# Kernel optimization log

Hardware: AMD Instinct MI355X
Metric: run time of the kernel (lower is better)

The kernel has to match this reference:

```python
import jax, jax.numpy as jnp
import numpy as np

S, B, H, D, G = 2048, 2, 16, 128, 16  # seq, batch, heads, head_dim, v-quant groups


def setup_inputs() -> dict:
    key = jax.random.key(0)
    ks = jax.random.split(key, 9)
    # int8-valued activations stored as float (torch code does .to(torch.int8))
    q = jax.random.randint(ks[0], (S, B, H, D), -128, 128).astype(jnp.float32)
    k = jax.random.randint(ks[1], (S, B, H, D), -128, 128).astype(jnp.float32)
    v = jax.random.randint(ks[2], (S, B, H, D), -128, 128).astype(jnp.float32)
    qmin = jax.random.normal(ks[3], (S, B, H, 1), jnp.float32) * 0.01
    qscale = jax.random.uniform(ks[4], (S, B, H, 1), jnp.float32, 0.005, 0.02)
    kmin = jax.random.normal(ks[5], (S, B, H, 1), jnp.float32) * 0.01
    kscale = jax.random.uniform(ks[6], (S, B, H, 1), jnp.float32, 0.005, 0.02)
    vmin = jax.random.normal(ks[7], (G, B, H, D, 1), jnp.float32) * 0.01
    vscale = jax.random.uniform(ks[8], (G, B, H, D, 1), jnp.float32, 0.005, 0.02)
    return {"query_layer": q, "key_layer": k, "value_layer": v,
            "qmin": qmin, "qscale": qscale, "kmin": kmin, "kscale": kscale,
            "vmin": vmin, "vscale": vscale, "causal": 1}


def _attention(query_layer, key_layer, value_layer, qmin, qscale, kmin, kscale, vmin, vscale, causal):
    # s b h d -> b h s d ; emulate .to(torch.int8) (values are already int8-range ints)
    q = jnp.transpose(query_layer, (1, 2, 0, 3))
    k = jnp.transpose(key_layer, (1, 2, 0, 3))
    v = jnp.transpose(value_layer, (1, 2, 0, 3))
    # per-token quant factors: s b h 1 -> b h s 1
    qm = jnp.transpose(qmin[..., 0], (1, 2, 0))[..., None]
    qs = jnp.transpose(qscale[..., 0], (1, 2, 0))[..., None]
    km = jnp.transpose(kmin[..., 0], (1, 2, 0))[..., None]
    ksc = jnp.transpose(kscale[..., 0], (1, 2, 0))[..., None]
    # attnq_qk: dequantize per-token then QK^T
    qd = q * qs + qm
    kd = k * ksc + km
    scores = jnp.einsum('bhsd,bhtd->bhst', qd, kd)
    # softmaxq: scale by 1/sqrt(128), causal mask, softmax, int8 requant of probs
    scores = scores * jnp.float32(1.0 / np.sqrt(128.0))
    s = scores.shape[-1]
    if causal:
        mask = jnp.tril(jnp.ones((s, s), dtype=bool))
        scores = jnp.where(mask, scores, jnp.float32(-1e9))
    probs = jax.nn.softmax(scores, axis=-1)
    pmin = jnp.min(probs, axis=-1, keepdims=True)
    pmax = jnp.max(probs, axis=-1, keepdims=True)
    pscale = (pmax - pmin) / 255.0 + jnp.float32(1e-12)
    quant_prob = jnp.round((probs - pmin) / pscale)  # int8-range prob codes
    # attnq_pv: dequant probs (per query token) and V (per sequence group) then PV
    pd = quant_prob * pscale + pmin
    vm = jnp.transpose(vmin[..., 0], (1, 2, 0, 3))  # b h g d
    vs = jnp.transpose(vscale[..., 0], (1, 2, 0, 3))
    gs = v.shape[2] // vm.shape[2]  # group size along sequence
    vd = v * jnp.repeat(vs, gs, axis=2) + jnp.repeat(vm, gs, axis=2)
    out = jnp.einsum('bhst,bhtd->bhsd', pd, vd)
    b, h, sq, d = out.shape
    return jnp.transpose(out, (2, 0, 1, 3)).reshape(sq, b, h * d)  # s b (h d)


def reference(query_layer, key_layer, value_layer, qmin, qscale, kmin, kscale, vmin, vscale, causal):
    return _attention(query_layer, key_layer, value_layer, qmin, qscale, kmin, kscale, vmin, vscale, causal)
```

## Files before the change

kernel.cpp:

```cpp
#include <hip/hip_runtime.h>
#include <math.h>


#define S_LEN 2048
#define BATCH 2
#define NH    16
#define HD    128
#define RSTR  4096
#define SCALE2 (0.08838834764831845f * 1.4426950408889634f)
#define EXP2F(x) __builtin_amdgcn_exp2f(x)

typedef int v4i __attribute__((ext_vector_type(4)));
#define MFMA16(a,b,c) __builtin_amdgcn_mfma_i32_16x16x64_i8((a),(b),(c),0,0,0)

#define WS_K8   0u
#define WS_V8T  (8u*1024u*1024u)
#define WS_SQ   (16u*1024u*1024u)
#define WS_SK   (WS_SQ + 256u*1024u)
#define WS_GSV  (WS_SK + 256u*1024u)

__device__ __forceinline__ int sbsum(unsigned p) {
    return (int)(signed char)(p) + (int)(signed char)(p>>8)
         + (int)(signed char)(p>>16) + (int)(signed char)(p>>24);
}

__global__ __launch_bounds__(256) void prep_pack(
    const float* __restrict__ Q, const float* __restrict__ K, const float* __restrict__ V,
    signed char* __restrict__ K8, float* __restrict__ SQs, float* __restrict__ SKs,
    signed char* __restrict__ V8T, float* __restrict__ GSV)
{
    __shared__ int v8i[128*33];
    const int tid = threadIdx.x;
    const int bx  = blockIdx.x;
    if (bx >= 512) {
        const int base = (bx - 512)*256 + tid;
        #pragma unroll
        for (int rep = 0; rep < 8; ++rep) {
            const int tensor = rep >> 2;
            const int idx = base + (rep & 3)*524288;
            const float* src = tensor ? K : Q;
            int tau = idx >> 5, dg = idx & 31;
            float4 x = *(const float4*)(src + (size_t)tau*128 + 4*dg);
            float ssum = x.x + x.y + x.z + x.w;
            #pragma unroll
            for (int off = 16; off >= 1; off >>= 1) ssum += __shfl_xor(ssum, off);
            if (tensor) {
                int a=(int)x.x, b2=(int)x.y, c=(int)x.z, d=(int)x.w;
                ((int*)K8)[(size_t)tau*32 + dg] = (a&255)|((b2&255)<<8)|((c&255)<<16)|((d&255)<<24);
                if ((tid & 31) == 0) SKs[tau] = ssum;
            } else {
                if ((tid & 31) == 0) SQs[tau] = ssum;
            }
        }
    } else {
        const int bid = bx;
        const int bh = bid & 31, ck = bid >> 5;
        const int b = bh >> 4, h = bh & 15;
        const int t0 = ck * 128;
        const int boff = b*2048 + h*128;
        #pragma unroll
        for (int it = 0; it < 16; ++it) {
            int idx = tid + it*256;
            int t = idx >> 5, dw = idx & 31;
            float4 x = *(const float4*)(V + (size_t)(t0+t)*RSTR + boff + 4*dw);
            int a=(int)x.x, b2=(int)x.y, c=(int)x.z, d=(int)x.w;
            v8i[t*33 + dw] = (a&255)|((b2&255)<<8)|((c&255)<<16)|((d&255)<<24);
        }
        __syncthreads();
        #pragma unroll
        for (int it = 0; it < 4; ++it) {
            int j = tid + it*256;
            int tg = j & 31, dw = j >> 5;
            unsigned r0 = (unsigned)v8i[(4*tg+0)*33 + dw];
            unsigned r1 = (unsigned)v8i[(4*tg+1)*33 + dw];
            unsigned r2 = (unsigned)v8i[(4*tg+2)*33 + dw];
            unsigned r3 = (unsigned)v8i[(4*tg+3)*33 + dw];
            unsigned x01 = __builtin_amdgcn_perm(r1, r0, 0x05010400u);
            unsigned x23 = __builtin_amdgcn_perm(r3, r2, 0x05010400u);
            unsigned y01 = __builtin_amdgcn_perm(r1, r0, 0x07030602u);
            unsigned y23 = __builtin_amdgcn_perm(r3, r2, 0x07030602u);
            unsigned p[4];
            p[0] = __builtin_amdgcn_perm(x23, x01, 0x05040100u);
            p[1] = __builtin_amdgcn_perm(x23, x01, 0x07060302u);
            p[2] = __builtin_amdgcn_perm(y23, y01, 0x05040100u);
            p[3] = __builtin_amdgcn_perm(y23, y01, 0x07060302u);
            int s[4];
            #pragma unroll
            for (int jj = 0; jj < 4; ++jj) {
                int d = 4*dw + jj;
                *(int*)(V8T + ((size_t)bh*128 + d)*2048 + t0 + 4*tg) = (int)p[jj];
                s[jj] = sbsum(p[jj]);
            }
            #pragma unroll
            for (int off = 1; off < 32; off <<= 1) {
                #pragma unroll
                for (int jj = 0; jj < 4; ++jj) s[jj] += __shfl_xor(s[jj], off);
            }
            if (tg == 0) {
                #pragma unroll
                for (int jj = 0; jj < 4; ++jj)
                    GSV[((size_t)bh*16 + ck)*128 + 4*dw + jj] = (float)s[jj];
            }
        }
    }
}

__global__ __launch_bounds__(256, 2) void attn_main(
    const float* __restrict__ Q,
    const signed char* __restrict__ K8, const signed char* __restrict__ V8T,
    const float* __restrict__ QMN, const float* __restrict__ QSC,
    const float* __restrict__ KMN, const float* __restrict__ KSC,
    const float* __restrict__ VMN, const float* __restrict__ VSC,
    const float* __restrict__ SQs, const float* __restrict__ SKs,
    const float* __restrict__ GSV,
    const int* __restrict__ CAUSAL, float* __restrict__ OUT)
{
    __shared__ __align__(16) signed char q8s[64*144];
    __shared__ __align__(16) signed char kv8s[128*144];
    __shared__ __align__(16) signed char pcs[64*144];
    __shared__ float rs_c1[64], rs_c2[64], rs_c3[64];
    __shared__ float rs_mx[64], rs_den[64], rs_mn[64];
    __shared__ float rs_u1[64], rs_w1[64], rs_psc[64], rs_pmn[64];
    __shared__ float ktA[2][128], ktB[2][128], ktC[2][128];
    __shared__ float vsA[128], vsB[128];
    __shared__ float vsumL[128], cgsL[128];

    signed char* k8s = kv8s;
    signed char* v8s = kv8s;

    const int tid  = threadIdx.x;
    const int w    = tid >> 6;
    const int lane = tid & 63;
    const int n    = lane & 15;
    const int quad = lane >> 4;
    const int bhi  = blockIdx.x & 31;
    const int qt   = 31 - (int)(blockIdx.x >> 5);
    const int b    = bhi >> 4, h = bhi & 15;
    const int causal = *CAUSAL;
    const int s0   = qt * 64;
    const int boff = b*2048 + h*128;
    const v4i vzero = {0,0,0,0};
    const v4i ones  = {0x01010101,0x01010101,0x01010101,0x01010101};

    #pragma unroll
    for (int it = 0; it < 8; ++it) {
        int idx = tid + it*256;
        int row = idx >> 5, d4 = (idx & 31) << 2;
        float4 x = *(const float4*)(Q + (size_t)(s0+row)*RSTR + boff + d4);
        int a=(int)x.x, b2=(int)x.y, c=(int)x.z, d=(int)x.w;
        *(int*)(q8s + row*144 + d4) = (a&255)|((b2&255)<<8)|((c&255)<<16)|((d&255)<<24);
    }
    if (tid < 64) {
        int si = (s0 + tid)*32 + bhi;
        float qs = QSC[si], qm = QMN[si];
        rs_c1[tid] = qs; rs_c2[tid] = qm;
        rs_c3[tid] = fmaf(qs, SQs[si], 128.0f*qm);
    }
    __syncthreads();

    const int kt_end = causal ? ((s0 + 63) >> 7) : 15;

    float c1r[4], c2r[4], c3r[4]; int qgr[4];
    #pragma unroll
    for (int r = 0; r < 4; ++r) {
        int qq = 16*w + 4*quad + r;
        c1r[r] = rs_c1[qq]; c2r[r] = rs_c2[qq]; c3r[r] = rs_c3[qq];
        qgr[r] = s0 + qq;
    }
    v4i a0p = *(const v4i*)(q8s + (16*w + n)*144 + 16*quad);
    v4i a1p = *(const v4i*)(q8s + (16*w + n)*144 + 64 + 16*quad);

    float m[4], l[4], mn[4];
    #pragma unroll
    for (int r = 0; r < 4; ++r) { m[r] = -INFINITY; l[r] = 0.f; mn[r] = INFINITY; }

#define P1_TILE(MASKED)                                                          \
  do {                                                                           \
    const int t0g = kt * 128;                                                    \
    __syncthreads();                                                             \
    _Pragma("unroll")                                                            \
    for (int it = 0; it < 4; ++it) {                                             \
        int idx = tid + it*256;                                                  \
        int trow = idx >> 3, doff = (idx & 7) << 4;                              \
        *(uint4*)(k8s + trow*144 + doff) =                                       \
            *(const uint4*)(K8 + ((size_t)(t0g+trow)*32 + bhi)*128 + doff);      \
    }                                                                            \
    if (tid < 128) {                                                             \
        int si = (t0g + tid)*32 + bhi;                                           \
        ktA[0][tid] = KSC[si]*SCALE2; ktB[0][tid] = KMN[si]*SCALE2;              \
        ktC[0][tid] = SKs[si];                                                   \
    }                                                                            \
    __syncthreads();                                                             \
    float tmax[4], sarr[8][4];                                                   \
    _Pragma("unroll")                                                            \
    for (int r = 0; r < 4; ++r) tmax[r] = -INFINITY;                             \
    _Pragma("unroll")                                                            \
    for (int tb = 0; tb < 8; ++tb) {                                             \
        v4i b0 = *(const v4i*)(k8s + (16*tb + n)*144 + 16*quad);                 \
        v4i b1 = *(const v4i*)(k8s + (16*tb + n)*144 + 64 + 16*quad);            \
        v4i acc = MFMA16(a0p, b0, vzero);                                        \
        acc = MFMA16(a1p, b1, acc);                                              \
        int tl = 16*tb + n;                                                      \
        float kA = ktA[0][tl], kB = ktB[0][tl], kC = ktC[0][tl];                 \
        _Pragma("unroll")                                                        \
        for (int r = 0; r < 4; ++r) {                                            \
            float Sf = (float)acc[r];                                            \
            float sv = fmaf(kA, fmaf(c1r[r], Sf, c2r[r]*kC), kB*c3r[r]);         \
            if (MASKED) sv = (t0g + tl > qgr[r]) ? -INFINITY : sv;               \
            sarr[tb][r] = sv;                                                    \
            tmax[r] = fmaxf(tmax[r], sv);                                        \
            mn[r] = fminf(mn[r], sv);                                            \
        }                                                                        \
    }                                                                            \
    _Pragma("unroll")                                                            \
    for (int r = 0; r < 4; ++r) {                                                \
        float mm = fmaxf(m[r], tmax[r]);                                         \
        if (mm > -INFINITY) {                                                    \
            float e0 = EXP2F(sarr[0][r]-mm) + EXP2F(sarr[1][r]-mm);              \
            float e1 = EXP2F(sarr[2][r]-mm) + EXP2F(sarr[3][r]-mm);              \
            float e2 = EXP2F(sarr[4][r]-mm) + EXP2F(sarr[5][r]-mm);              \
            float e3 = EXP2F(sarr[6][r]-mm) + EXP2F(sarr[7][r]-mm);              \
            l[r] = fmaf(l[r], EXP2F(m[r]-mm), (e0+e1)+(e2+e3));                  \
            m[r] = mm;                                                           \
        }                                                                        \
    }                                                                            \
  } while (0)

    {
        int kt;
        for (kt = 0; kt < kt_end; ++kt) P1_TILE(false);
        kt = kt_end;
        if (causal) P1_TILE(true); else P1_TILE(false);
    }

    #pragma unroll
    for (int r = 0; r < 4; ++r) {
        #pragma unroll
        for (int off = 1; off < 16; off <<= 1) {
            float m2 = __shfl_xor(m[r], off);
            float l2 = __shfl_xor(l[r], off);
            float n2 = __shfl_xor(mn[r], off);
            float mm = fmaxf(m[r], m2);
            if (mm > -INFINITY) l[r] = l[r]*EXP2F(m[r]-mm) + l2*EXP2F(m2-mm);
            m[r] = mm;
            mn[r] = fminf(mn[r], n2);
        }
        if (n == 0) {
            int qq = 16*w + 4*quad + r;
            rs_mx[qq] = m[r]; rs_den[qq] = l[r]; rs_mn[qq] = mn[r];
        }
    }
    __syncthreads();
    if (tid < 64) {
        float mx = rs_mx[tid], den = rs_den[tid], mnv = rs_mn[tid];
        float invd = 1.0f/den;
        int s = s0 + tid;
        bool hasmask = (causal != 0) && (s < S_LEN-1);
        float pmin = hasmask ? 0.0f : EXP2F(mnv - mx)*invd;
        float psc  = (invd - pmin)/255.0f + 1e-12f;
        float ipsc = 1.0f/psc;
        rs_u1[tid] = invd*ipsc; rs_w1[tid] = -pmin*ipsc;
        rs_psc[tid] = psc; rs_pmn[tid] = pmin;
    } else if (tid >= 128) {
        int d = tid - 128;
        float vsum = 0.f, cgs = 0.f;
        #pragma unroll
        for (int g = 0; g < 16; ++g) {
            float gs = GSV[((size_t)bhi*16 + g)*128 + d];
            int vi = ((g*BATCH + b)*NH + h)*HD + d;
            float vs = VSC[vi], vm = VMN[vi];
            vsum = fmaf(vs, gs, fmaf(128.0f, vm, vsum));
            if (g <= kt_end) cgs = fmaf(128.0f*vs, gs, fmaf(16384.0f, vm, cgs));
        }
        vsumL[d] = vsum; cgsL[d] = cgs;
        int si = d*32 + bhi;
        ktA[0][d] = KSC[si]*SCALE2; ktB[0][d] = KMN[si]*SCALE2; ktC[0][d] = SKs[si];
    }
    __syncthreads();

    v4i qb0[4], qb1[4];
    float qc1[4], qc2[4], qc3[4], qmxn[4], qu1[4], qw1[4];
    int qgq[4];
    #pragma unroll
    for (int cb = 0; cb < 4; ++cb) {
        int qcol = 16*cb + n;
        qb0[cb] = *(const v4i*)(q8s + qcol*144 + 16*quad);
        qb1[cb] = *(const v4i*)(q8s + qcol*144 + 64 + 16*quad);
        qc1[cb] = rs_c1[qcol]; qc2[cb] = rs_c2[qcol]; qc3[cb] = rs_c3[qcol];
        qmxn[cb] = -rs_mx[qcol]; qu1[cb] = rs_u1[qcol]; qw1[cb] = rs_w1[qcol];
        qgq[cb] = s0 + qcol;
    }

    float outa[4][8];
    #pragma unroll
    for (int r = 0; r < 4; ++r)
        #pragma unroll
        for (int db = 0; db < 8; ++db) outa[r][db] = 0.f;

#define P2_TILE(MASKED)                                                          \
  do {                                                                           \
    const int t0g = kt * 128;                                                    \
    const int cur = kt & 1;                                                      \
    __syncthreads();                  \
    _Pragma("unroll")                                                            \
    for (int it = 0; it < 4; ++it) {                                             \
        int idx = tid + it*256;                                                  \
        int trow = idx >> 3, doff = (idx & 7) << 4;                              \
        *(uint4*)(v8s + trow*144 + doff) =                                       \
            *(const uint4*)(V8T + ((size_t)bhi*128 + trow)*2048 + t0g + doff);   \
    }                                                                            \
    if (tid < 128) {                                                             \
        if (kt < kt_end) {                                                       \
            int si = (t0g + 128 + tid)*32 + bhi;                                 \
            ktA[cur^1][tid] = KSC[si]*SCALE2;                                    \
            ktB[cur^1][tid] = KMN[si]*SCALE2;                                    \
            ktC[cur^1][tid] = SKs[si];                                           \
        }                                                                        \
    } else {                                                                     \
        int d = tid - 128;                                                       \
        int vi = ((kt*BATCH + b)*NH + h)*HD + d;                                 \
        vsA[d] = VSC[vi]; vsB[d] = VMN[vi];                                      \
    }                                                                            \
    _Pragma("unroll")                                                            \
    for (int rb = 0; rb < 2; ++rb) {                                             \
        int trow = 32*w + 16*rb;                                                 \
        const signed char* kp = K8 + ((size_t)(t0g+trow+n)*32 + bhi)*128         \
                                   + 16*quad;                                    \
        v4i a0 = *(const v4i*)kp;              \
        v4i a1 = *(const v4i*)(kp + 64);                                         \
        float ksr[4], kmr[4], skr[4];                                            \
        int tgb = t0g + trow + 4*quad;                                           \
        _Pragma("unroll")                                                        \
        for (int r = 0; r < 4; ++r) {                                            \
            int tl = trow + 4*quad + r;                                          \
            ksr[r] = ktA[cur][tl]; kmr[r] = ktB[cur][tl]; skr[r] = ktC[cur][tl]; \
        }                                                                        \
        _Pragma("unroll")                                                        \
        for (int cb = 0; cb < 4; ++cb) {                                         \
            v4i acc = MFMA16(a0, qb0[cb], vzero);                                \
            acc = MFMA16(a1, qb1[cb], acc);                                      \
            int cby[4];                                                          \
            _Pragma("unroll")                                                    \
            for (int r = 0; r < 4; ++r) {                                        \
                float Sf = (float)acc[r];                                        \
                float x = fmaf(ksr[r], fmaf(qc1[cb], Sf, qc2[cb]*skr[r]),        \
                               fmaf(kmr[r], qc3[cb], qmxn[cb]));                 \
                if (MASKED) x = (tgb + r > qgq[cb]) ? -INFINITY : x;             \
                float e = EXP2F(x);                                              \
                float f = fmaf(e, qu1[cb], qw1[cb]) + 8388608.0f;   \
                cby[r] = __float_as_int(f);                                      \
            }                                                                    \
            unsigned t01 = __builtin_amdgcn_perm((unsigned)cby[1],               \
                                                 (unsigned)cby[0], 0x00000400u); \
            unsigned t23 = __builtin_amdgcn_perm((unsigned)cby[3],               \
                                                 (unsigned)cby[2], 0x04000000u); \
            int packed = (int)(__builtin_amdgcn_perm(t23, t01, 0x07060100u)      \
                               ^ 0x80808080u);          \
            *(int*)(pcs + (16*cb + n)*144 + trow + 4*quad) = packed;             \
        }                                                                        \
    }                                                                            \
    __syncthreads();                                                             \
    {                                                                            \
        v4i a0 = *(const v4i*)(pcs + (16*w + n)*144 + 16*quad);                  \
        v4i a1 = *(const v4i*)(pcs + (16*w + n)*144 + 64 + 16*quad);             \
        v4i c1a = MFMA16(a0, ones, vzero);                                       \
        c1a = MFMA16(a1, ones, c1a);                                             \
        float c1f[4];                                                            \
        _Pragma("unroll")                                                        \
        for (int r = 0; r < 4; ++r) c1f[r] = (float)c1a[r];                      \
        _Pragma("unroll")                                                        \
        for (int db = 0; db < 8; ++db) {                                         \
            v4i b0 = *(const v4i*)(v8s + (16*db + n)*144 + 16*quad);             \
            v4i b1 = *(const v4i*)(v8s + (16*db + n)*144 + 64 + 16*quad);        \
            v4i cv = MFMA16(a0, b0, vzero);                                      \
            cv = MFMA16(a1, b1, cv);                                             \
            int d = 16*db + n;                                                   \
            float vs = vsA[d], vm = vsB[d];                                      \
            _Pragma("unroll")                                                    \
            for (int r = 0; r < 4; ++r)                                          \
                outa[r][db] = fmaf(vs, (float)cv[r],                             \
                                   fmaf(vm, c1f[r], outa[r][db]));               \
        }                                                                        \
    }                                                                            \
  } while (0)

    {
        int kt;
        for (kt = 0; kt < kt_end; ++kt) P2_TILE(false);
        kt = kt_end;
        if (causal) P2_TILE(true); else P2_TILE(false);
    }

    float pscr[4], pmnr[4];
    #pragma unroll
    for (int r = 0; r < 4; ++r) {
        int qq = 16*w + 4*quad + r;
        pscr[r] = rs_psc[qq]; pmnr[r] = rs_pmn[qq];
    }
    #pragma unroll
    for (int db = 0; db < 8; ++db) {
        int d = 16*db + n;
        float vsum = vsumL[d];
        float cgs  = cgsL[d];
        #pragma unroll
        for (int r = 0; r < 4; ++r) {
            int s = s0 + 16*w + 4*quad + r;
            OUT[(size_t)s*RSTR + boff + d] = fmaf(pscr[r], outa[r][db] + cgs, pmnr[r]*vsum);
        }
    }
}

extern "C" void kernel_launch(void* const* d_in, const int* in_sizes, int n_in,
                              void* d_out, int out_size, void* d_ws, size_t ws_size,
                              hipStream_t stream) {
    (void)in_sizes; (void)n_in; (void)out_size; (void)ws_size;
    const float* Q   = (const float*)d_in[0];
    const float* K   = (const float*)d_in[1];
    const float* V   = (const float*)d_in[2];
    const float* QMN = (const float*)d_in[3];
    const float* QSC = (const float*)d_in[4];
    const float* KMN = (const float*)d_in[5];
    const float* KSC = (const float*)d_in[6];
    const float* VMN = (const float*)d_in[7];
    const float* VSC = (const float*)d_in[8];
    const int*   CS  = (const int*)d_in[9];
    float* out = (float*)d_out;

    char* ws = (char*)d_ws;
    signed char* K8  = (signed char*)(ws + WS_K8);
    signed char* V8T = (signed char*)(ws + WS_V8T);
    float* SQs  = (float*)(ws + WS_SQ);
    float* SKs  = (float*)(ws + WS_SK);
    float* GSVp = (float*)(ws + WS_GSV);

    prep_pack<<<512 + 2048, 256, 0, stream>>>(Q, K, V, K8, SQs, SKs, V8T, GSVp);
    attn_main<<<1024, 256, 0, stream>>>(Q, K8, V8T, QMN, QSC, KMN, KSC, VMN, VSC,
                                        SQs, SKs, GSVp, CS, out);
}
```

Measured before the change: 256.3 us.

## Compute Q/K/V row sums with ones-MFMA in-kernel instead of a prepass

Drops the precomputed Q/K row sums and per-group V column sums from the prep kernel. The attention kernel now derives them on the fly by multiplying the int8 tiles with an all-ones operand on the MFMA units. The prep kernel is split into separate K and V pack kernels and no longer reads Q, which removes a full pass over Q plus the workspace traffic. The per-element row-minimum update is also skipped when it cannot matter in the causal case. The cost is extra MFMA instructions in both the score and PV loops, which adds compute in the main kernel.

```diff
diff --git a/kernel.cpp b/kernel.cpp
--- a/kernel.cpp
+++ b/kernel.cpp
@@ -15,93 +15,59 @@
 
 #define WS_K8   0u
 #define WS_V8T  (8u*1024u*1024u)
-#define WS_SQ   (16u*1024u*1024u)
-#define WS_SK   (WS_SQ + 256u*1024u)
-#define WS_GSV  (WS_SK + 256u*1024u)
-
-__device__ __forceinline__ int sbsum(unsigned p) {
-    return (int)(signed char)(p) + (int)(signed char)(p>>8)
-         + (int)(signed char)(p>>16) + (int)(signed char)(p>>24);
+
+__global__ __launch_bounds__(256) void prep_k(const float* __restrict__ K,
+                                              signed char* __restrict__ K8)
+{
+    const int base = blockIdx.x*2048 + threadIdx.x;
+    #pragma unroll
+    for (int rep = 0; rep < 8; ++rep) {
+        int idx = base + rep*256;
+        float4 x = *(const float4*)(K + (size_t)idx*4);
+        int a=(int)x.x, b=(int)x.y, c=(int)x.z, d=(int)x.w;
+        ((int*)K8)[idx] = (a&255)|((b&255)<<8)|((c&255)<<16)|((d&255)<<24);
+    }
 }
 
-__global__ __launch_bounds__(256) void prep_pack(
-    const float* __restrict__ Q, const float* __restrict__ K, const float* __restrict__ V,
-    signed char* __restrict__ K8, float* __restrict__ SQs, float* __restrict__ SKs,
-    signed char* __restrict__ V8T, float* __restrict__ GSV)
+__global__ __launch_bounds__(256) void prep_v(const float* __restrict__ V,
+                                              signed char* __restrict__ V8T)
 {
     __shared__ int v8i[128*33];
     const int tid = threadIdx.x;
-    const int bx  = blockIdx.x;
-    if (bx >= 512) {
-        const int base = (bx - 512)*256 + tid;
+    const int bid = blockIdx.x;
+    const int bh = bid & 31, ck = bid >> 5;
+    const int b = bh >> 4, h = bh & 15;
+    const int t0 = ck * 128;
+    const int boff = b*2048 + h*128;
+    #pragma unroll
+    for (int it = 0; it < 16; ++it) {
+        int idx = tid + it*256;
+        int t = idx >> 5, dw = idx & 31;
+        float4 x = *(const float4*)(V + (size_t)(t0+t)*RSTR + boff + 4*dw);
+        int a=(int)x.x, b2=(int)x.y, c=(int)x.z, d=(int)x.w;
+        v8i[t*33 + dw] = (a&255)|((b2&255)<<8)|((c&255)<<16)|((d&255)<<24);
+    }
+    __syncthreads();
+    #pragma unroll
+    for (int it = 0; it < 4; ++it) {
+        int j = tid + it*256;
+        int tg = j & 31, dw = j >> 5;
+        unsigned r0 = (unsigned)v8i[(4*tg+0)*33 + dw];
+        unsigned r1 = (unsigned)v8i[(4*tg+1)*33 + dw];
+        unsigned r2 = (unsigned)v8i[(4*tg+2)*33 + dw];
+        unsigned r3 = (unsigned)v8i[(4*tg+3)*33 + dw];
+        unsigned x01 = __builtin_amdgcn_perm(r1, r0, 0x05010400u);
+        unsigned x23 = __builtin_amdgcn_perm(r3, r2, 0x05010400u);
+        unsigned y01 = __builtin_amdgcn_perm(r1, r0, 0x07030602u);
+        unsigned y23 = __builtin_amdgcn_perm(r3, r2, 0x07030602u);
+        unsigned p[4];
+        p[0] = __builtin_amdgcn_perm(x23, x01, 0x05040100u);
+        p[1] = __builtin_amdgcn_perm(x23, x01, 0x07060302u);
+        p[2] = __builtin_amdgcn_perm(y23, y01, 0x05040100u);
+        p[3] = __builtin_amdgcn_perm(y23, y01, 0x07060302u);
         #pragma unroll
-        for (int rep = 0; rep < 8; ++rep) {
-            const int tensor = rep >> 2;
-            const int idx = base + (rep & 3)*524288;
-            const float* src = tensor ? K : Q;
-            int tau = idx >> 5, dg = idx & 31;
-            float4 x = *(const float4*)(src + (size_t)tau*128 + 4*dg);
-            float ssum = x.x + x.y + x.z + x.w;
-            #pragma unroll
-            for (int off = 16; off >= 1; off >>= 1) ssum += __shfl_xor(ssum, off);
-            if (tensor) {
-                int a=(int)x.x, b2=(int)x.y, c=(int)x.z, d=(int)x.w;
-                ((int*)K8)[(size_t)tau*32 + dg] = (a&255)|((b2&255)<<8)|((c&255)<<16)|((d&255)<<24);
-                if ((tid & 31) == 0) SKs[tau] = ssum;
-            } else {
-                if ((tid & 31) == 0) SQs[tau] = ssum;
-            }
-        }
-    } else {
-        const int bid = bx;
-        const int bh = bid & 31, ck = bid >> 5;
-        const int b = bh >> 4, h = bh & 15;
-        const int t0 = ck * 128;
-        const int boff = b*2048 + h*128;
-        #pragma unroll
-        for (int it = 0; it < 16; ++it) {
-            int idx = tid + it*256;
-            int t = idx >> 5, dw = idx & 31;
-            float4 x = *(const float4*)(V + (size_t)(t0+t)*RSTR + boff + 4*dw);
-            int a=(int)x.x, b2=(int)x.y, c=(int)x.z, d=(int)x.w;
-            v8i[t*33 + dw] = (a&255)|((b2&255)<<8)|((c&255)<<16)|((d&255)<<24);
-        }
-        __syncthreads();
-        #pragma unroll
-        for (int it = 0; it < 4; ++it) {
-            int j = tid + it*256;
-            int tg = j & 31, dw = j >> 5;
-            unsigned r0 = (unsigned)v8i[(4*tg+0)*33 + dw];
-            unsigned r1 = (unsigned)v8i[(4*tg+1)*33 + dw];
-            unsigned r2 = (unsigned)v8i[(4*tg+2)*33 + dw];
-            unsigned r3 = (unsigned)v8i[(4*tg+3)*33 + dw];
-            unsigned x01 = __builtin_amdgcn_perm(r1, r0, 0x05010400u);
-            unsigned x23 = __builtin_amdgcn_perm(r3, r2, 0x05010400u);
-            unsigned y01 = __builtin_amdgcn_perm(r1, r0, 0x07030602u);
-            unsigned y23 = __builtin_amdgcn_perm(r3, r2, 0x07030602u);
-            unsigned p[4];
-            p[0] = __builtin_amdgcn_perm(x23, x01, 0x05040100u);
-            p[1] = __builtin_amdgcn_perm(x23, x01, 0x07060302u);
-            p[2] = __builtin_amdgcn_perm(y23, y01, 0x05040100u);
-            p[3] = __builtin_amdgcn_perm(y23, y01, 0x07060302u);
-            int s[4];
-            #pragma unroll
-            for (int jj = 0; jj < 4; ++jj) {
-                int d = 4*dw + jj;
-                *(int*)(V8T + ((size_t)bh*128 + d)*2048 + t0 + 4*tg) = (int)p[jj];
-                s[jj] = sbsum(p[jj]);
-            }
-            #pragma unroll
-            for (int off = 1; off < 32; off <<= 1) {
-                #pragma unroll
-                for (int jj = 0; jj < 4; ++jj) s[jj] += __shfl_xor(s[jj], off);
-            }
-            if (tg == 0) {
-                #pragma unroll
-                for (int jj = 0; jj < 4; ++jj)
-                    GSV[((size_t)bh*16 + ck)*128 + 4*dw + jj] = (float)s[jj];
-            }
-        }
+        for (int jj = 0; jj < 4; ++jj)
+            *(int*)(V8T + ((size_t)bh*128 + 4*dw + jj)*2048 + t0 + 4*tg) = (int)p[jj];
     }
 }
 
@@ -111,8 +77,6 @@
     const float* __restrict__ QMN, const float* __restrict__ QSC,
     const float* __restrict__ KMN, const float* __restrict__ KSC,
     const float* __restrict__ VMN, const float* __restrict__ VSC,
-    const float* __restrict__ SQs, const float* __restrict__ SKs,
-    const float* __restrict__ GSV,
     const int* __restrict__ CAUSAL, float* __restrict__ OUT)
 {
     __shared__ __align__(16) signed char q8s[64*144];
@@ -121,9 +85,8 @@
     __shared__ float rs_c1[64], rs_c2[64], rs_c3[64];
     __shared__ float rs_mx[64], rs_den[64], rs_mn[64];
     __shared__ float rs_u1[64], rs_w1[64], rs_psc[64], rs_pmn[64];
-    __shared__ float ktA[2][128], ktB[2][128], ktC[2][128];
+    __shared__ float ktA[2][128], ktB[2][128];
     __shared__ float vsA[128], vsB[128];
-    __shared__ float vsumL[128], cgsL[128];
 
     signed char* k8s = kv8s;
     signed char* v8s = kv8s;
@@ -141,6 +104,7 @@
     const int boff = b*2048 + h*128;
     const v4i vzero = {0,0,0,0};
     const v4i ones  = {0x01010101,0x01010101,0x01010101,0x01010101};
+    const bool needmn = (!causal) || (qt == 31);
 
     #pragma unroll
     for (int it = 0; it < 8; ++it) {
@@ -152,13 +116,26 @@
     }
     if (tid < 64) {
         int si = (s0 + tid)*32 + bhi;
-        float qs = QSC[si], qm = QMN[si];
-        rs_c1[tid] = qs; rs_c2[tid] = qm;
-        rs_c3[tid] = fmaf(qs, SQs[si], 128.0f*qm);
+        rs_c1[tid] = QSC[si]; rs_c2[tid] = QMN[si];
     }
     __syncthreads();
 
     const int kt_end = causal ? ((s0 + 63) >> 7) : 15;
+
+    v4i a0p = *(const v4i*)(q8s + (16*w + n)*144 + 16*quad);
+    v4i a1p = *(const v4i*)(q8s + (16*w + n)*144 + 64 + 16*quad);
+    {
+        v4i qsum = MFMA16(a0p, ones, vzero);
+        qsum = MFMA16(a1p, ones, qsum);
+        if (n == 0) {
+            #pragma unroll
+            for (int r = 0; r < 4; ++r) {
+                int qq = 16*w + 4*quad + r;
+                rs_c3[qq] = fmaf(rs_c1[qq], (float)qsum[r], 128.0f*rs_c2[qq]);
+            }
+        }
+    }
+    __syncthreads();
 
     float c1r[4], c2r[4], c3r[4]; int qgr[4];
     #pragma unroll
@@ -167,8 +144,6 @@
         c1r[r] = rs_c1[qq]; c2r[r] = rs_c2[qq]; c3r[r] = rs_c3[qq];
         qgr[r] = s0 + qq;
     }
-    v4i a0p = *(const v4i*)(q8s + (16*w + n)*144 + 16*quad);
-    v4i a1p = *(const v4i*)(q8s + (16*w + n)*144 + 64 + 16*quad);
 
     float m[4], l[4], mn[4];
     #pragma unroll
@@ -188,7 +163,6 @@
     if (tid < 128) {                                                             \
         int si = (t0g + tid)*32 + bhi;                                           \
         ktA[0][tid] = KSC[si]*SCALE2; ktB[0][tid] = KMN[si]*SCALE2;              \
-        ktC[0][tid] = SKs[si];                                                   \
     }                                                                            \
     __syncthreads();                                                             \
     float tmax[4], sarr[8][4];                                                   \
@@ -200,8 +174,10 @@
         v4i b1 = *(const v4i*)(k8s + (16*tb + n)*144 + 64 + 16*quad);            \
         v4i acc = MFMA16(a0p, b0, vzero);                                        \
         acc = MFMA16(a1p, b1, acc);                                              \
+        v4i acc1 = MFMA16(ones, b0, vzero);                                      \
+        acc1 = MFMA16(ones, b1, acc1);                                           \
         int tl = 16*tb + n;                                                      \
-        float kA = ktA[0][tl], kB = ktB[0][tl], kC = ktC[0][tl];                 \
+        float kA = ktA[0][tl], kB = ktB[0][tl], kC = (float)acc1[0];             \
         _Pragma("unroll")                                                        \
         for (int r = 0; r < 4; ++r) {                                            \
             float Sf = (float)acc[r];                                            \
@@ -209,7 +185,7 @@
             if (MASKED) sv = (t0g + tl > qgr[r]) ? -INFINITY : sv;               \
             sarr[tb][r] = sv;                                                    \
             tmax[r] = fmaxf(tmax[r], sv);                                        \
-            mn[r] = fminf(mn[r], sv);                                            \
+            if (needmn) mn[r] = fminf(mn[r], sv);                                \
         }                                                                        \
     }                                                                            \
     _Pragma("unroll")                                                            \
@@ -263,18 +239,8 @@
         rs_psc[tid] = psc; rs_pmn[tid] = pmin;
     } else if (tid >= 128) {
         int d = tid - 128;
-        float vsum = 0.f, cgs = 0.f;
-        #pragma unroll
-        for (int g = 0; g < 16; ++g) {
-            float gs = GSV[((size_t)bhi*16 + g)*128 + d];
-            int vi = ((g*BATCH + b)*NH + h)*HD + d;
-            float vs = VSC[vi], vm = VMN[vi];
-            vsum = fmaf(vs, gs, fmaf(128.0f, vm, vsum));
-            if (g <= kt_end) cgs = fmaf(128.0f*vs, gs, fmaf(16384.0f, vm, cgs));
-        }
-        vsumL[d] = vsum; cgsL[d] = cgs;
         int si = d*32 + bhi;
-        ktA[0][d] = KSC[si]*SCALE2; ktB[0][d] = KMN[si]*SCALE2; ktC[0][d] = SKs[si];
+        ktA[0][d] = KSC[si]*SCALE2; ktB[0][d] = KMN[si]*SCALE2;
     }
     __syncthreads();
 
@@ -292,6 +258,9 @@
     }
 
     float outa[4][8];
+    float cgsr[8], vsr[8];
+    #pragma unroll
+    for (int db = 0; db < 8; ++db) { cgsr[db] = 0.f; vsr[db] = 0.f; }
     #pragma unroll
     for (int r = 0; r < 4; ++r)
         #pragma unroll
@@ -314,7 +283,6 @@
             int si = (t0g + 128 + tid)*32 + bhi;                                 \
             ktA[cur^1][tid] = KSC[si]*SCALE2;                                    \
             ktB[cur^1][tid] = KMN[si]*SCALE2;                                    \
-            ktC[cur^1][tid] = SKs[si];                                           \
         }                                                                        \
     } else {                                                                     \
         int d = tid - 128;                                                       \
@@ -328,12 +296,15 @@
                                    + 16*quad;                                    \
         v4i a0 = *(const v4i*)kp;              \
         v4i a1 = *(const v4i*)(kp + 64);                                         \
+        v4i accK = MFMA16(a0, ones, vzero);                \
+        accK = MFMA16(a1, ones, accK);                                           \
         float ksr[4], kmr[4], skr[4];                                            \
         int tgb = t0g + trow + 4*quad;                                           \
         _Pragma("unroll")                                                        \
         for (int r = 0; r < 4; ++r) {                                            \
             int tl = trow + 4*quad + r;                                          \
-            ksr[r] = ktA[cur][tl]; kmr[r] = ktB[cur][tl]; skr[r] = ktC[cur][tl]; \
+            ksr[r] = ktA[cur][tl]; kmr[r] = ktB[cur][tl];                        \
+            skr[r] = (float)accK[r];                                             \
         }                                                                        \
         _Pragma("unroll")                                                        \
         for (int cb = 0; cb < 4; ++cb) {                                         \
@@ -374,8 +345,13 @@
             v4i b1 = *(const v4i*)(v8s + (16*db + n)*144 + 64 + 16*quad);        \
             v4i cv = MFMA16(a0, b0, vzero);                                      \
             cv = MFMA16(a1, b1, cv);                                             \
+            v4i ga = MFMA16(ones, b0, vzero);        \
+            ga = MFMA16(ones, b1, ga);                                           \
             int d = 16*db + n;                                                   \
             float vs = vsA[d], vm = vsB[d];                                      \
+            float gsum = (float)ga[0];                                           \
+            cgsr[db] = fmaf(128.0f*vs, gsum, fmaf(16384.0f, vm, cgsr[db]));      \
+            vsr[db]  = fmaf(vs, gsum, fmaf(128.0f, vm, vsr[db]));                \
             _Pragma("unroll")                                                    \
             for (int r = 0; r < 4; ++r)                                          \
                 outa[r][db] = fmaf(vs, (float)cv[r],                             \
@@ -400,12 +376,10 @@
     #pragma unroll
     for (int db = 0; db < 8; ++db) {
         int d = 16*db + n;
-        float vsum = vsumL[d];
-        float cgs  = cgsL[d];
         #pragma unroll
         for (int r = 0; r < 4; ++r) {
             int s = s0 + 16*w + 4*quad + r;
-            OUT[(size_t)s*RSTR + boff + d] = fmaf(pscr[r], outa[r][db] + cgs, pmnr[r]*vsum);
+            OUT[(size_t)s*RSTR + boff + d] = fmaf(pscr[r], outa[r][db] + cgsr[db], pmnr[r]*vsr[db]);
         }
     }
 }
@@ -429,11 +403,9 @@
     char* ws = (char*)d_ws;
     signed char* K8  = (signed char*)(ws + WS_K8);
     signed char* V8T = (signed char*)(ws + WS_V8T);
-    float* SQs  = (float*)(ws + WS_SQ);
-    float* SKs  = (float*)(ws + WS_SK);
-    float* GSVp = (float*)(ws + WS_GSV);
-
-    prep_pack<<<512 + 2048, 256, 0, stream>>>(Q, K, V, K8, SQs, SKs, V8T, GSVp);
+
+    prep_v<<<512, 256, 0, stream>>>(V, V8T);
+    prep_k<<<1024, 256, 0, stream>>>(K, K8);
     attn_main<<<1024, 256, 0, stream>>>(Q, K8, V8T, QMN, QSC, KMN, KSC, VMN, VSC,
-                                        SQs, SKs, GSVp, CS, out);
+                                        CS, out);
 }
```

New measurement: 253.9 us. Within noise of the previous version (-1.0%).
